# Kernel optimization log

Hardware: AMD Instinct MI355X
Metric: run time of the kernel (lower is better)

The kernel has to match this reference:

```python
import jax, jax.numpy as jnp
import numpy as np

D_MODEL = 1024
H = 16
D_K = D_MODEL // H  # 64
RANK = 5
ALPHA = 1.0


def _lora_linear(x, W, b, dW, dB):
    # merged weight: W + alpha * dB @ dW  (shape [out, in]); F.linear -> x @ W_merged.T + b
    Wm = W + ALPHA * (dB @ dW)
    return x @ Wm.T + b


def setup_inputs() -> dict:
    key = jax.random.key(0)
    ks = jax.random.split(key, 16)
    b_s, nq = 2, 2048
    s = 1.0 / np.sqrt(D_MODEL).astype(np.float32)
    inp = {
        "x": jax.random.normal(ks[0], (b_s, nq, D_MODEL), dtype=jnp.float32),
    }
    names = ["q", "k", "v", "o"]
    i = 1
    for n in names:
        inp[f"{n}_w"] = jax.random.normal(ks[i], (D_MODEL, D_MODEL), dtype=jnp.float32) * s; i += 1
        inp[f"{n}_b"] = jnp.zeros((D_MODEL,), dtype=jnp.float32)
        inp[f"{n}_dw"] = jax.random.normal(ks[i], (RANK, D_MODEL), dtype=jnp.float32) * 0.01; i += 1
        inp[f"{n}_db"] = jax.random.normal(ks[i], (D_MODEL, RANK), dtype=jnp.float32) * 0.01; i += 1
    return inp


def reference(x, q_w, q_b, q_dw, q_db, k_w, k_b, k_dw, k_db,
              v_w, v_b, v_dw, v_db, o_w, o_b, o_dw, o_db):
    b_s, nq, _ = x.shape
    q = _lora_linear(x, q_w, q_b, q_dw, q_db).reshape(b_s, nq, H, D_K)
    k = _lora_linear(x, k_w, k_b, k_dw, k_db).reshape(b_s, nq, H, D_K)
    v = _lora_linear(x, v_w, v_b, v_dw, v_db).reshape(b_s, nq, H, D_K)
    # scores: [b, h, q, k]
    att = jnp.einsum("bqhd,bkhd->bhqk", q, k) / np.sqrt(D_K).astype(np.float32)
    att = jax.nn.softmax(att, axis=-1)
    out = jnp.einsum("bhqk,bkhd->bqhd", att, v).reshape(b_s, nq, H * D_K)
    out = _lora_linear(out, o_w, o_b, o_dw, o_db)
    return out
```

## Files before the change

kernel.cpp:

```cpp
#include <hip/hip_runtime.h>
#include <hip/hip_bf16.h>

#define NQ 2048
#define NB 2

typedef unsigned short u16;
typedef unsigned int u32;
typedef _Float16 f16;
typedef __attribute__((ext_vector_type(8))) _Float16 half8;
typedef __attribute__((ext_vector_type(2))) __fp16 fp16x2;
typedef __attribute__((ext_vector_type(4))) float f32x4;
typedef __attribute__((ext_vector_type(2))) unsigned int u32x2;

#define MFMAH(A, B, C) __builtin_amdgcn_mfma_f32_16x16x32_f16(A, B, C, 0, 0, 0)

__device__ __forceinline__ u16 f2h(float x) {
    f16 h = (f16)x;
    return *(u16*)&h;
}
__device__ __forceinline__ u32 pk_h2(float a, float b) {
    union { fp16x2 v; u32 u; } c;
    c.v = __builtin_amdgcn_cvt_pkrtz(a, b);
    return c.u;
}
__device__ __forceinline__ float fexp2(float x) {
#if __has_builtin(__builtin_amdgcn_exp2f)
    return __builtin_amdgcn_exp2f(x);
#else
    return exp2f(x);
#endif
}
__device__ __forceinline__ void glds16(const u16* g, u16* l) {
    typedef const __attribute__((address_space(1))) u16 gu16;
    typedef __attribute__((address_space(3))) u16 lu16;
    __builtin_amdgcn_global_load_lds((gu16*)g, (lu16*)l, 16, 0, 0);
}
__device__ __forceinline__ void pl32swap(u32& a, u32& b) {
#if __has_builtin(__builtin_amdgcn_permlane32_swap)
    u32x2 r = __builtin_amdgcn_permlane32_swap(a, b, false, false);
    a = r[0]; b = r[1];
#else
    asm volatile("v_permlane32_swap_b32 %0, %1" : "+v"(a), "+v"(b));
#endif
}
__device__ __forceinline__ void pl16swap(u32& a, u32& b) {
#if __has_builtin(__builtin_amdgcn_permlane16_swap)
    u32x2 r = __builtin_amdgcn_permlane16_swap(a, b, false, false);
    a = r[0]; b = r[1];
#else
    asm volatile("v_permlane16_swap_b32 %0, %1" : "+v"(a), "+v"(b));
#endif
}

#define QSCALE 0.18033688011112042f

__global__ __launch_bounds__(256) void merge_w16(
    const float* __restrict__ w0, const float* __restrict__ dw0, const float* __restrict__ db0,
    const float* __restrict__ w1, const float* __restrict__ dw1, const float* __restrict__ db1,
    const float* __restrict__ w2, const float* __restrict__ dw2, const float* __restrict__ db2,
    const float* __restrict__ w3, const float* __restrict__ dw3, const float* __restrict__ db3,
    u16* __restrict__ Wf) {
    int i4 = (blockIdx.x * 256 + threadIdx.x) * 4;
    int row = i4 >> 10, col = i4 & 1023;
    int which = row >> 10, lr = row & 1023;
    const float* W  = (which == 0) ? w0  : (which == 1) ? w1  : (which == 2) ? w2  : w3;
    const float* dW = (which == 0) ? dw0 : (which == 1) ? dw1 : (which == 2) ? dw2 : dw3;
    const float* dB = (which == 0) ? db0 : (which == 1) ? db1 : (which == 2) ? db2 : db3;
    float4 acc = *(const float4*)&W[lr * 1024 + col];
#pragma unroll
    for (int r = 0; r < 5; ++r) {
        float s = dB[lr * 5 + r];
        float4 w4 = *(const float4*)&dW[r * 1024 + col];
        acc.x += s * w4.x; acc.y += s * w4.y;
        acc.z += s * w4.z; acc.w += s * w4.w;
    }
    if (which == 0) { acc.x *= QSCALE; acc.y *= QSCALE; acc.z *= QSCALE; acc.w *= QSCALE; }
    ushort4 o = make_ushort4(f2h(acc.x), f2h(acc.y), f2h(acc.z), f2h(acc.w));
    *(ushort4*)&Wf[i4] = o;
}

__global__ __launch_bounds__(256) void bias_pack(
    const float* __restrict__ b0, const float* __restrict__ b1,
    const float* __restrict__ b2, const float* __restrict__ b3,
    float* __restrict__ ball) {
    int t = blockIdx.x * 256 + threadIdx.x;
    int which = t >> 10;
    const float* B = (which == 0) ? b0 : (which == 1) ? b1 : (which == 2) ? b2 : b3;
    float v = B[t & 1023];
    if (which == 0) v *= QSCALE;
    ball[t] = v;
}

__global__ __launch_bounds__(256) void xcast(const float* __restrict__ x,
                                             u16* __restrict__ xf) {
    int i4 = (blockIdx.x * 256 + threadIdx.x) * 4;
    float4 v = *(const float4*)&x[i4];
    *(uint2*)&xf[i4] = make_uint2(pk_h2(v.x, v.y), pk_h2(v.z, v.w));
}

template <int TM>
__global__ __launch_bounds__(256) void gemm_f16(
    const u16* __restrict__ Af, const u16* __restrict__ Bf,
    const float* __restrict__ bias,
    float* __restrict__ Cf, u16* __restrict__ Cb, int ldc,
    u16* __restrict__ VtOut) {
    constexpr int MI = TM / 32;
    __shared__ u16 As[2][TM * 32];
    __shared__ u16 Bs[2][128 * 32];
    const int tid = threadIdx.x;
    const int wid = tid >> 6, lane = tid & 63;
    const int ln = lane & 15, quad = lane >> 4;
    const int bm = blockIdx.y * TM, bn = blockIdx.x * 128;
    const int wm = (wid >> 1) * (TM / 2), wn = (wid & 1) * 64;
    const int lrow = lane >> 2;
    const int lchunk = (lane & 3) * 8;

    f32x4 acc[MI][4];
#pragma unroll
    for (int i = 0; i < MI; ++i)
#pragma unroll
        for (int j = 0; j < 4; ++j) acc[i][j] = (f32x4){0.f, 0.f, 0.f, 0.f};

    for (int k0 = 0; k0 < 1024; k0 += 64) {
#pragma unroll
        for (int hf = 0; hf < 2; ++hf) {
#pragma unroll
            for (int p = 0; p < TM / 64; ++p) {
                int r = p * 64 + wid * 16;
                glds16(&Af[(bm + r + lrow) * 1024 + k0 + hf * 32 + lchunk],
                       &As[hf][r * 32]);
            }
#pragma unroll
            for (int p = 0; p < 2; ++p) {
                int r = p * 64 + wid * 16;
                glds16(&Bf[(bn + r + lrow) * 1024 + k0 + hf * 32 + lchunk],
                       &Bs[hf][r * 32]);
            }
        }
        asm volatile("s_waitcnt vmcnt(0)" ::: "memory");
        __syncthreads();

        half8 a[MI][2], b[4][2];
#pragma unroll
        for (int kc = 0; kc < 2; ++kc) {
#pragma unroll
            for (int j = 0; j < 4; ++j)
                b[j][kc] = *(const half8*)&Bs[kc][(wn + j * 16 + ln) * 32 + quad * 8];
#pragma unroll
            for (int i = 0; i < MI; ++i)
                a[i][kc] = *(const half8*)&As[kc][(wm + i * 16 + ln) * 32 + quad * 8];
        }
#pragma unroll
        for (int i = 0; i < MI; ++i)
#pragma unroll
            for (int j = 0; j < 4; ++j) {
                acc[i][j] = MFMAH(a[i][0], b[j][0], acc[i][j]);
                acc[i][j] = MFMAH(a[i][1], b[j][1], acc[i][j]);
            }
        __syncthreads();
    }

    if (VtOut && bn >= 2048) {
#pragma unroll
        for (int i = 0; i < MI; ++i)
#pragma unroll
            for (int j = 0; j < 4; ++j) {
                int col = bn + wn + j * 16 + ln;
                float bv = bias[col];
                int colV = col - 2048;
                int row0 = bm + wm + i * 16 + quad * 4;
                ushort4 pk = make_ushort4(f2h(acc[i][j][0] + bv), f2h(acc[i][j][1] + bv),
                                          f2h(acc[i][j][2] + bv), f2h(acc[i][j][3] + bv));
                *(ushort4*)&VtOut[colV * 4096 + row0] = pk;
            }
        return;
    }

#pragma unroll
    for (int i = 0; i < MI; ++i)
#pragma unroll
        for (int j = 0; j < 4; ++j) {
            int col = bn + wn + j * 16 + ln;
            float bv = bias[col];
#pragma unroll
            for (int r = 0; r < 4; ++r) {
                int row = bm + wm + i * 16 + quad * 4 + r;
                float v = acc[i][j][r] + bv;
                if (Cb) Cb[row * ldc + col] = f2h(v);
                else    Cf[row * ldc + col] = v;
            }
        }
}

__global__ __launch_bounds__(256) void flash_f16(
    const u16* __restrict__ QKV, const u16* __restrict__ Vt,
    u16* __restrict__ AO) {
    __shared__ u16 Ks[2][2][64 * 32];
    __shared__ u16 Vs[2][2][64 * 32];

    const int tid = threadIdx.x;
    const int wid = tid >> 6, lane = tid & 63;
    const int ln = lane & 15, quad = lane >> 4;
    const int qt = blockIdx.x, h = blockIdx.y, b = blockIdx.z;
    const int rowbase = b * NQ;
    const int col0 = h * 64;
    const int q0 = rowbase + qt * 128 + wid * 32;
    const int lrow = lane >> 2;
    const int kchunk = ((lane & 3) ^ ((lrow >> 1) & 3)) * 8;
    const int kswz = (quad ^ ((ln >> 1) & 3)) * 8;

    const half8 ones = {(f16)1, (f16)1, (f16)1, (f16)1,
                        (f16)1, (f16)1, (f16)1, (f16)1};

    half8 qf[2][2];
#pragma unroll
    for (int mi = 0; mi < 2; ++mi)
#pragma unroll
        for (int kc = 0; kc < 2; ++kc)
            qf[mi][kc] = *(const half8*)&QKV[(q0 + mi * 16 + ln) * 3072 + col0 +
                                             kc * 32 + quad * 8];

    f32x4 accO[4][2];
    f32x4 accS[2];
#pragma unroll
    for (int mi = 0; mi < 2; ++mi) {
        accS[mi] = (f32x4){0.f, 0.f, 0.f, 0.f};
#pragma unroll
        for (int a = 0; a < 4; ++a) accO[a][mi] = (f32x4){0.f, 0.f, 0.f, 0.f};
    }

    const int NT = NQ / 64;
    const u16* Kg = QKV + (rowbase + wid * 16 + lrow) * 3072 + 1024 + col0 + kchunk;
    const u16* Vg = Vt + (col0 + wid * 16 + lrow) * 4096 + rowbase + kchunk;

#define STAGE(kt2, bu)                                         \
    {                                                          \
        const u16* kg_ = Kg + (kt2) * (64 * 3072);             \
        const u16* vg_ = Vg + (kt2) * 64;                      \
        glds16(kg_,      &Ks[bu][0][wid * 512]);               \
        glds16(kg_ + 32, &Ks[bu][1][wid * 512]);               \
        glds16(vg_,      &Vs[bu][0][wid * 512]);               \
        glds16(vg_ + 32, &Vs[bu][1][wid * 512]);               \
    }

    STAGE(0, 0);
    asm volatile("s_waitcnt vmcnt(0)" ::: "memory");
    __syncthreads();

#pragma unroll 2
    for (int kt = 0; kt < NT; ++kt) {
        const int cur = kt & 1;
        if (kt + 1 < NT) STAGE(kt + 1, cur ^ 1);

        f32x4 s[4][2];
#pragma unroll
        for (int a = 0; a < 4; ++a) {
            half8 kf0 = *(const half8*)&Ks[cur][0][(a * 16 + ln) * 32 + kswz];
            half8 kf1 = *(const half8*)&Ks[cur][1][(a * 16 + ln) * 32 + kswz];
#pragma unroll
            for (int mi = 0; mi < 2; ++mi) {
                f32x4 t = (f32x4){0.f, 0.f, 0.f, 0.f};
                t = MFMAH(kf0, qf[mi][0], t);
                t = MFMAH(kf1, qf[mi][1], t);
                s[a][mi] = t;
            }
        }

        half8 pf[2][2];
#pragma unroll
        for (int mi = 0; mi < 2; ++mi)
#pragma unroll
            for (int kc = 0; kc < 2; ++kc) {
                u32 c0 = pk_h2(fexp2(s[2 * kc][mi][0]), fexp2(s[2 * kc][mi][1]));
                u32 c1 = pk_h2(fexp2(s[2 * kc][mi][2]), fexp2(s[2 * kc][mi][3]));
                u32 c2 = pk_h2(fexp2(s[2 * kc + 1][mi][0]), fexp2(s[2 * kc + 1][mi][1]));
                u32 c3 = pk_h2(fexp2(s[2 * kc + 1][mi][2]), fexp2(s[2 * kc + 1][mi][3]));
                pl32swap(c0, c2);
                pl32swap(c1, c3);
                pl16swap(c0, c2);
                pl16swap(c1, c3);
                union { u32 u[4]; half8 h; } pu;
                pu.u[0] = c0; pu.u[1] = c1; pu.u[2] = c2; pu.u[3] = c3;
                pf[mi][kc] = pu.h;
                accS[mi] = MFMAH(ones, pf[mi][kc], accS[mi]);
            }

#pragma unroll
        for (int a = 0; a < 4; ++a) {
            half8 vf0 = *(const half8*)&Vs[cur][0][(a * 16 + ln) * 32 + kswz];
            half8 vf1 = *(const half8*)&Vs[cur][1][(a * 16 + ln) * 32 + kswz];
#pragma unroll
            for (int mi = 0; mi < 2; ++mi) {
                accO[a][mi] = MFMAH(vf0, pf[mi][0], accO[a][mi]);
                accO[a][mi] = MFMAH(vf1, pf[mi][1], accO[a][mi]);
            }
        }

        asm volatile("s_waitcnt vmcnt(0)" ::: "memory");
        __syncthreads();
    }
#undef STAGE

#pragma unroll
    for (int mi = 0; mi < 2; ++mi) {
        float inv = 1.f / accS[mi][0];
        int q = q0 + mi * 16 + ln;
#pragma unroll
        for (int a = 0; a < 4; ++a) {
            ushort4 pk = make_ushort4(f2h(accO[a][mi][0] * inv),
                                      f2h(accO[a][mi][1] * inv),
                                      f2h(accO[a][mi][2] * inv),
                                      f2h(accO[a][mi][3] * inv));
            *(ushort4*)&AO[q * 1024 + col0 + a * 16 + quad * 4] = pk;
        }
    }
}

extern "C" void kernel_launch(void* const* d_in, const int* in_sizes, int n_in,
                              void* d_out, int out_size, void* d_ws, size_t ws_size,
                              hipStream_t stream) {
    const float* x = (const float*)d_in[0];
    const float* w[4]  = {(const float*)d_in[1],  (const float*)d_in[5],
                          (const float*)d_in[9],  (const float*)d_in[13]};
    const float* bv[4] = {(const float*)d_in[2],  (const float*)d_in[6],
                          (const float*)d_in[10], (const float*)d_in[14]};
    const float* dw[4] = {(const float*)d_in[3],  (const float*)d_in[7],
                          (const float*)d_in[11], (const float*)d_in[15]};
    const float* db[4] = {(const float*)d_in[4],  (const float*)d_in[8],
                          (const float*)d_in[12], (const float*)d_in[16]};

    u16* p = (u16*)d_ws;
    u16* Wf  = p; p += 4096 * 1024;
    u16* xf  = p; p += 4096 * 1024;
    u16* QKV = p; p += 4096 * 3072;
    u16* Vt  = p; p += 1024 * 4096;
    float* ball = (float*)p;
    u16* AO = xf;

    merge_w16<<<4096, 256, 0, stream>>>(w[0], dw[0], db[0], w[1], dw[1], db[1],
                                        w[2], dw[2], db[2], w[3], dw[3], db[3], Wf);
    bias_pack<<<16, 256, 0, stream>>>(bv[0], bv[1], bv[2], bv[3], ball);
    xcast<<<4096, 256, 0, stream>>>(x, xf);

    gemm_f16<128><<<dim3(24, 32), 256, 0, stream>>>(xf, Wf, ball,
                                                    nullptr, QKV, 3072, Vt);

    flash_f16<<<dim3(NQ / 128, 16, NB), 256, 0, stream>>>(QKV, Vt, AO);

    gemm_f16<64><<<dim3(8, 64), 256, 0, stream>>>(AO, Wf + 3072 * 1024,
                                                  ball + 3072, (float*)d_out, nullptr, 1024,
                                                  nullptr);
}
```

Before: 227.8 us.

## Software-pipeline attention loop: overlap QK^T/exp of next tile with PV of previous

Splits K and V staging into separate loads and restructures the flash-attention loop so QK^T+exp for tile k+1 is issued alongside the PV MFMAs for tile k, with V loaded one tile behind K. The goal is to give the scheduler independent MFMA and exp work to interleave, hiding exp/VALU latency and LDS reads behind matrix ops. It costs extra registers for a second P fragment set and a more complex prologue/epilogue, which may reduce occupancy.

```diff
diff --git a/kernel.cpp b/kernel.cpp
--- a/kernel.cpp
+++ b/kernel.cpp
@@ -233,30 +233,25 @@
     const u16* Kg = QKV + (rowbase + wid * 16 + lrow) * 3072 + 1024 + col0 + kchunk;
     const u16* Vg = Vt + (col0 + wid * 16 + lrow) * 4096 + rowbase + kchunk;
 
-#define STAGE(kt2, bu)                                         \
+#define STAGEK(kt2, bu)                                        \
     {                                                          \
         const u16* kg_ = Kg + (kt2) * (64 * 3072);             \
-        const u16* vg_ = Vg + (kt2) * 64;                      \
         glds16(kg_,      &Ks[bu][0][wid * 512]);               \
         glds16(kg_ + 32, &Ks[bu][1][wid * 512]);               \
+    }
+#define STAGEV(kt2, bu)                                        \
+    {                                                          \
+        const u16* vg_ = Vg + (kt2) * 64;                      \
         glds16(vg_,      &Vs[bu][0][wid * 512]);               \
         glds16(vg_ + 32, &Vs[bu][1][wid * 512]);               \
     }
 
-    STAGE(0, 0);
-    asm volatile("s_waitcnt vmcnt(0)" ::: "memory");
-    __syncthreads();
-
-#pragma unroll 2
-    for (int kt = 0; kt < NT; ++kt) {
-        const int cur = kt & 1;
-        if (kt + 1 < NT) STAGE(kt + 1, cur ^ 1);
-
+    auto qk_exp = [&](int kb, half8 (&pf)[2][2]) {
         f32x4 s[4][2];
 #pragma unroll
         for (int a = 0; a < 4; ++a) {
-            half8 kf0 = *(const half8*)&Ks[cur][0][(a * 16 + ln) * 32 + kswz];
-            half8 kf1 = *(const half8*)&Ks[cur][1][(a * 16 + ln) * 32 + kswz];
+            half8 kf0 = *(const half8*)&Ks[kb][0][(a * 16 + ln) * 32 + kswz];
+            half8 kf1 = *(const half8*)&Ks[kb][1][(a * 16 + ln) * 32 + kswz];
 #pragma unroll
             for (int mi = 0; mi < 2; ++mi) {
                 f32x4 t = (f32x4){0.f, 0.f, 0.f, 0.f};
@@ -265,8 +260,6 @@
                 s[a][mi] = t;
             }
         }
-
-        half8 pf[2][2];
 #pragma unroll
         for (int mi = 0; mi < 2; ++mi)
 #pragma unroll
@@ -284,22 +277,55 @@
                 pf[mi][kc] = pu.h;
                 accS[mi] = MFMAH(ones, pf[mi][kc], accS[mi]);
             }
-
+    };
+
+    auto pv = [&](const half8 (&pf)[2][2], int vb) {
 #pragma unroll
         for (int a = 0; a < 4; ++a) {
-            half8 vf0 = *(const half8*)&Vs[cur][0][(a * 16 + ln) * 32 + kswz];
-            half8 vf1 = *(const half8*)&Vs[cur][1][(a * 16 + ln) * 32 + kswz];
+            half8 vf0 = *(const half8*)&Vs[vb][0][(a * 16 + ln) * 32 + kswz];
+            half8 vf1 = *(const half8*)&Vs[vb][1][(a * 16 + ln) * 32 + kswz];
 #pragma unroll
             for (int mi = 0; mi < 2; ++mi) {
                 accO[a][mi] = MFMAH(vf0, pf[mi][0], accO[a][mi]);
                 accO[a][mi] = MFMAH(vf1, pf[mi][1], accO[a][mi]);
             }
         }
-
+    };
+
+    half8 pfA[2][2], pfB[2][2];
+
+    STAGEK(0, 0);
+    STAGEV(0, 0);
+    asm volatile("s_waitcnt vmcnt(0)" ::: "memory");
+    __syncthreads();
+    STAGEK(1, 1);
+    qk_exp(0, pfA);
+    asm volatile("s_waitcnt vmcnt(0)" ::: "memory");
+    __syncthreads();
+
+    for (int kt = 0; kt < NT - 2; kt += 2) {
+        STAGEK(kt + 2, 0);
+        STAGEV(kt + 1, 1);
+        qk_exp(1, pfB);
+        pv(pfA, 0);
         asm volatile("s_waitcnt vmcnt(0)" ::: "memory");
         __syncthreads();
-    }
-#undef STAGE
+
+        STAGEK(kt + 3, 1);
+        STAGEV(kt + 2, 0);
+        qk_exp(0, pfA);
+        pv(pfB, 1);
+        asm volatile("s_waitcnt vmcnt(0)" ::: "memory");
+        __syncthreads();
+    }
+    STAGEV(NT - 1, 1);
+    qk_exp(1, pfB);
+    pv(pfA, 0);
+    asm volatile("s_waitcnt vmcnt(0)" ::: "memory");
+    __syncthreads();
+    pv(pfB, 1);
+#undef STAGEK
+#undef STAGEV
 
 #pragma unroll
     for (int mi = 0; mi < 2; ++mi) {
```

Result: no change. 226.1 us (-0.8%).
